# Optimization experiments

Hardware: AMD Instinct MI355X
Metric: run time of the kernel (lower is better)

Reference implementation:

```python
import jax, jax.numpy as jnp
import numpy as np

B, S, H = 2, 1024, 2048
NH, NKV, HD = 16, 4, 128
E, TOPK, I = 8, 2, 768
EPS = 1e-6
ROPE_THETA = 1000000.0


def setup_inputs() -> dict:
    key = jax.random.key(0)
    ks = jax.random.split(key, 14)
    sc = 0.02
    hidden_states = jax.random.normal(ks[0], (B, S, H), jnp.float32)
    # rotary embeddings (HF-style: cos/sin of shape [B, S, head_dim])
    pos = jnp.arange(S, dtype=jnp.float32)
    inv_freq = 1.0 / (ROPE_THETA ** (jnp.arange(0, HD, 2, dtype=jnp.float32) / HD))
    freqs = pos[:, None] * inv_freq[None, :]            # [S, HD/2]
    emb = jnp.concatenate([freqs, freqs], axis=-1)      # [S, HD]
    cos = jnp.broadcast_to(jnp.cos(emb)[None], (B, S, HD))
    sin = jnp.broadcast_to(jnp.sin(emb)[None], (B, S, HD))
    # additive causal mask [B, 1, S, S]
    causal = jnp.tril(jnp.ones((S, S), bool))
    attention_mask = jnp.broadcast_to(
        jnp.where(causal, 0.0, -1e9).astype(jnp.float32)[None, None], (B, 1, S, S))
    params = dict(
        w_q=jax.random.normal(ks[1], (NH * HD, H), jnp.float32) * sc,
        w_k=jax.random.normal(ks[2], (NKV * HD, H), jnp.float32) * sc,
        w_v=jax.random.normal(ks[3], (NKV * HD, H), jnp.float32) * sc,
        w_o=jax.random.normal(ks[4], (H, NH * HD), jnp.float32) * sc,
        q_norm_w=jnp.ones((HD,), jnp.float32),
        k_norm_w=jnp.ones((HD,), jnp.float32),
        ln1_w=jnp.ones((H,), jnp.float32),
        ln2_w=jnp.ones((H,), jnp.float32),
        gate_w=jax.random.normal(ks[5], (E, H), jnp.float32) * sc,
        w_gate_e=jax.random.normal(ks[6], (E, I, H), jnp.float32) * sc,
        w_up_e=jax.random.normal(ks[7], (E, I, H), jnp.float32) * sc,
        w_down_e=jax.random.normal(ks[8], (E, H, I), jnp.float32) * sc,
    )
    return dict(hidden_states=hidden_states, start_pos=0, cos=cos, sin=sin,
                attention_mask=attention_mask, **params)


def _rmsnorm(x, w):
    return x * jax.lax.rsqrt(jnp.mean(x * x, axis=-1, keepdims=True) + EPS) * w


def _rotate_half(x):
    x1, x2 = jnp.split(x, 2, axis=-1)
    return jnp.concatenate([-x2, x1], axis=-1)


def reference(hidden_states, start_pos, cos, sin, attention_mask,
              w_q, w_k, w_v, w_o, q_norm_w, k_norm_w, ln1_w, ln2_w,
              gate_w, w_gate_e, w_up_e, w_down_e):
    b, s, h = hidden_states.shape
    # ---- attention block ----
    x = _rmsnorm(hidden_states, ln1_w)
    q = _rmsnorm((x @ w_q.T).reshape(b, s, NH, HD), q_norm_w)
    k = _rmsnorm((x @ w_k.T).reshape(b, s, NKV, HD), k_norm_w)
    v = (x @ w_v.T).reshape(b, s, NKV, HD)
    c, sn = cos[:, :, None, :], sin[:, :, None, :]
    q = q * c + _rotate_half(q) * sn
    k = k * c + _rotate_half(k) * sn
    # GQA: repeat kv heads (start_pos=0 -> cache holds only current keys/values)
    rep = NH // NKV
    k = jnp.repeat(k, rep, axis=2)
    v = jnp.repeat(v, rep, axis=2)
    scale = HD ** -0.5
    scores = jnp.einsum('bqhd,bkhd->bhqk', q, k) * scale + attention_mask
    attn = jax.nn.softmax(scores, axis=-1)
    ctx = jnp.einsum('bhqk,bkhd->bqhd', attn, v).reshape(b, s, NH * HD)
    hidden_states = hidden_states + ctx @ w_o.T
    # ---- sparse MoE block ----
    x2 = _rmsnorm(hidden_states, ln2_w).reshape(-1, h)          # [T, H]
    logits = x2 @ gate_w.T                                      # [T, E]
    probs = jax.nn.softmax(logits.astype(jnp.float32), axis=-1)
    topw, topi = jax.lax.top_k(probs, TOPK)                     # [T, K]
    topw = topw / jnp.sum(topw, axis=-1, keepdims=True)         # norm_topk_prob
    # combine weights [T, E]: nonzero only on selected experts -> same math as
    # the original gather/scatter dispatch, expressed densely.
    cw = jnp.sum(jax.nn.one_hot(topi, E, dtype=x2.dtype) * topw[..., None], axis=1)
    g = jnp.einsum('th,eih->tei', x2, w_gate_e)                 # [T, E, I]
    u = jnp.einsum('th,eih->tei', x2, w_up_e)
    act = jax.nn.silu(g) * u
    moe_out = jnp.einsum('tei,ehi->th', act * cw[:, :, None], w_down_e)
    return hidden_states + moe_out.reshape(b, s, h)
```

## Files before the change

kernel.cpp:

```cpp
#include <hip/hip_runtime.h>


namespace {

constexpr int cB = 2, cS = 1024, cH = 2048;
constexpr int cNH = 16, cNKV = 4, cHD = 128;
constexpr int cE = 8, cI = 768;
constexpr int cT = cB * cS;
constexpr int cDq = cNH * cHD;
constexpr int cDkv = cNKV * cHD;
constexpr float cEPS = 1e-6f;
constexpr float cSCALE = 0.08838834764831845f;
constexpr int cQT = cS / 64;

typedef __attribute__((ext_vector_type(8))) short bf16x8;
typedef __attribute__((ext_vector_type(4))) float f32x4;

__device__ __forceinline__ unsigned pack2(float f0, float f1) {
  unsigned u0 = __float_as_uint(f0), u1 = __float_as_uint(f1);
  unsigned r0 = (u0 + (0x7FFFu + ((u0 >> 16) & 1u))) >> 16;
  unsigned r1 = (u1 + (0x7FFFu + ((u1 >> 16) & 1u))) & 0xFFFF0000u;
  return r0 | r1;
}
__device__ __forceinline__ uint4 pack8(const float4& a, const float4& b) {
  return make_uint4(pack2(a.x, a.y), pack2(a.z, a.w),
                    pack2(b.x, b.y), pack2(b.z, b.w));
}

__device__ __forceinline__ unsigned pack2t(float f0, float f1) {
  return (__float_as_uint(f0) >> 16) | (__float_as_uint(f1) & 0xFFFF0000u);
}
__device__ __forceinline__ float hi_of(float f) {
  return __uint_as_float(__float_as_uint(f) & 0xFFFF0000u);
}
__device__ __forceinline__ void split8(const float4& x, const float4& y,
                                       uint4& h, uint4& l) {
  h = make_uint4(pack2t(x.x, x.y), pack2t(x.z, x.w),
                 pack2t(y.x, y.y), pack2t(y.z, y.w));
  float l0 = x.x - hi_of(x.x), l1 = x.y - hi_of(x.y);
  float l2 = x.z - hi_of(x.z), l3 = x.w - hi_of(x.w);
  float l4 = y.x - hi_of(y.x), l5 = y.y - hi_of(y.y);
  float l6 = y.z - hi_of(y.z), l7 = y.w - hi_of(y.w);
  l = make_uint4(pack2t(l0, l1), pack2t(l2, l3), pack2t(l4, l5), pack2t(l6, l7));
}

__global__ __launch_bounds__(256) void k_rmsnorm(
    const float* __restrict__ xin, const float* __restrict__ w,
    float* __restrict__ y) {
  int t = blockIdx.x, tid = threadIdx.x;
  __shared__ float red[256];
  const float* xr = xin + (size_t)t * cH;
  float xv[8];
  float ss = 0.f;
#pragma unroll
  for (int i = 0; i < 8; ++i) {
    xv[i] = xr[tid + i * 256];
    ss += xv[i] * xv[i];
  }
  red[tid] = ss;
  __syncthreads();
  for (int s = 128; s > 0; s >>= 1) {
    if (tid < s) red[tid] += red[tid + s];
    __syncthreads();
  }
  float inv = rsqrtf(red[0] / (float)cH + cEPS);
#pragma unroll
  for (int i = 0; i < 8; ++i)
    y[(size_t)t * cH + tid + i * 256] = xv[i] * inv * w[tid + i * 256];
}

#define SGEMM_BODY(APTR_EXPR, WPTR_EXPR, KDIM, EPILOGUE)                      \
  __shared__ __align__(16) short Ah[128 * 32];                                \
  __shared__ __align__(16) short Al[128 * 32];                                \
  __shared__ __align__(16) short Bh[128 * 32];                                \
  __shared__ __align__(16) short Bl[128 * 32];                                \
  int tid = threadIdx.x;                                                      \
  int sdst[2];                                                                \
  const float* aptr[2];                                                       \
  const float* wptr[2];                                                       \
  _Pragma("unroll") for (int b2 = 0; b2 < 2; ++b2) {                          \
    int bid = tid + b2 * 256;                                                 \
    int row = bid >> 2, blk = bid & 3;                                        \
    sdst[b2] = row * 4 + (blk ^ ((row >> 1) & 3));                            \
    aptr[b2] = (APTR_EXPR) + blk * 8;                                         \
    wptr[b2] = (WPTR_EXPR) + blk * 8;                                         \
  }                                                                           \
  int w = tid >> 6, l = tid & 63;                                             \
  int wr = (w >> 1) * 64, wc = (w & 1) * 64;                                  \
  int sub = l >> 4, l16 = l & 15;                                             \
  int offA[4], offB[4];                                                       \
  _Pragma("unroll") for (int i = 0; i < 4; ++i) {                             \
    int ra = wr + i * 16 + l16;                                               \
    offA[i] = ra * 4 + (sub ^ ((ra >> 1) & 3));                               \
    int rb = wc + i * 16 + l16;                                               \
    offB[i] = rb * 4 + (sub ^ ((rb >> 1) & 3));                               \
  }                                                                           \
  f32x4 acc[4][4] = {};                                                       \
  uint4* Ah4 = (uint4*)Ah;                                                    \
  uint4* Al4 = (uint4*)Al;                                                    \
  uint4* Bh4 = (uint4*)Bh;                                                    \
  uint4* Bl4 = (uint4*)Bl;                                                    \
  const bf16x8* Ahf = (const bf16x8*)Ah;                                      \
  const bf16x8* Alf = (const bf16x8*)Al;                                      \
  const bf16x8* Bhf = (const bf16x8*)Bh;                                      \
  const bf16x8* Blf = (const bf16x8*)Bl;                                      \
  for (int k0 = 0; k0 < (KDIM); k0 += 32) {                                   \
    float4 av0[2], av1[2], wv0[2], wv1[2];                                    \
    _Pragma("unroll") for (int b2 = 0; b2 < 2; ++b2) {                        \
      av0[b2] = *(const float4*)(aptr[b2] + k0);                              \
      av1[b2] = *(const float4*)(aptr[b2] + k0 + 4);                          \
      wv0[b2] = *(const float4*)(wptr[b2] + k0);                              \
      wv1[b2] = *(const float4*)(wptr[b2] + k0 + 4);                          \
    }                                                                         \
    __syncthreads();                                                          \
    _Pragma("unroll") for (int b2 = 0; b2 < 2; ++b2) {                        \
      uint4 h, lo;                                                            \
      split8(av0[b2], av1[b2], h, lo);                                        \
      Ah4[sdst[b2]] = h;                                                      \
      Al4[sdst[b2]] = lo;                                                     \
      split8(wv0[b2], wv1[b2], h, lo);                                        \
      Bh4[sdst[b2]] = h;                                                      \
      Bl4[sdst[b2]] = lo;                                                     \
    }                                                                         \
    __syncthreads();                                                          \
    bf16x8 ah[4], al[4], bh[4], bl[4];                                        \
    _Pragma("unroll") for (int i = 0; i < 4; ++i) {                           \
      ah[i] = Ahf[offA[i]];                                                   \
      al[i] = Alf[offA[i]];                                                   \
    }                                                                         \
    _Pragma("unroll") for (int j = 0; j < 4; ++j) {                           \
      bh[j] = Bhf[offB[j]];                                                   \
      bl[j] = Blf[offB[j]];                                                   \
    }                                                                         \
    _Pragma("unroll") for (int i = 0; i < 4; ++i)                             \
        _Pragma("unroll") for (int j = 0; j < 4; ++j) {                       \
      acc[i][j] = __builtin_amdgcn_mfma_f32_16x16x32_bf16(ah[i], bh[j],       \
                                                          acc[i][j], 0, 0, 0);\
      acc[i][j] = __builtin_amdgcn_mfma_f32_16x16x32_bf16(al[i], bh[j],       \
                                                          acc[i][j], 0, 0, 0);\
      acc[i][j] = __builtin_amdgcn_mfma_f32_16x16x32_bf16(ah[i], bl[j],       \
                                                          acc[i][j], 0, 0, 0);\
    }                                                                         \
  }                                                                           \
  _Pragma("unroll") for (int i = 0; i < 4; ++i) {                             \
    _Pragma("unroll") for (int rr = 0; rr < 4; ++rr) {                        \
      int lr = wr + i * 16 + sub * 4 + rr;                                    \
      _Pragma("unroll") for (int j = 0; j < 4; ++j) {                         \
        int nn = wc + j * 16 + l16;                                           \
        float vv = acc[i][j][rr];                                             \
        EPILOGUE;                                                             \
      }                                                                       \
    }                                                                         \
  }

__global__ __launch_bounds__(256, 2) void k_sgemm_qkv(
    const float* __restrict__ A, const float* __restrict__ Wq,
    const float* __restrict__ Wk, const float* __restrict__ Wv,
    float* __restrict__ Cq, float* __restrict__ Ck, float* __restrict__ Cv) {
  int nBase = blockIdx.x * 128;
  int mBase = blockIdx.y * 128;
  const float* W;
  float* C;
  int Nout, ncol;
  if (nBase < cDq) {
    W = Wq; C = Cq; Nout = cDq; ncol = nBase;
  } else if (nBase < cDq + cDkv) {
    W = Wk; C = Ck; Nout = cDkv; ncol = nBase - cDq;
  } else {
    W = Wv; C = Cv; Nout = cDkv; ncol = nBase - cDq - cDkv;
  }
  SGEMM_BODY(A + (size_t)(mBase + row) * cH,
             W + (size_t)(ncol + row) * cH, cH,
             C[(size_t)(mBase + lr) * Nout + ncol + nn] = vv)
}

__global__ __launch_bounds__(256, 2) void k_sgemm_o(
    const float* __restrict__ A, const float* __restrict__ W,
    float* __restrict__ C, const float* __restrict__ resid) {
  int nBase = blockIdx.x * 128;
  int mBase = blockIdx.y * 128;
  SGEMM_BODY(A + (size_t)(mBase + row) * cH,
             W + (size_t)(nBase + row) * cH, cH,
             {
               size_t idx = (size_t)(mBase + lr) * cH + nBase + nn;
               C[idx] = vv + resid[idx];
             })
}

__global__ __launch_bounds__(128) void k_qknorm_rope(
    float* qbuf, float* kbuf,
    const float* __restrict__ qw, const float* __restrict__ kw,
    const float* __restrict__ cosb, const float* __restrict__ sinb,
    int cosBS) {
  int t = blockIdx.x, head = blockIdx.y, d = threadIdx.x;
  float* buf;
  const float* w;
  if (head < cNH) {
    buf = qbuf + (size_t)t * cDq + head * cHD;
    w = qw;
  } else {
    buf = kbuf + (size_t)t * cDkv + (head - cNH) * cHD;
    w = kw;
  }
  __shared__ float xs[cHD];
  __shared__ float red[cHD];
  float x = buf[d];
  xs[d] = x;
  red[d] = x * x;
  __syncthreads();
  for (int s = 64; s > 0; s >>= 1) {
    if (d < s) red[d] += red[d + s];
    __syncthreads();
  }
  float inv = rsqrtf(red[0] / (float)cHD + cEPS);
  int od = d ^ 64;
  float y = x * inv * w[d];
  float yo = xs[od] * inv * w[od];
  float rot = (d < 64) ? -yo : yo;
  size_t ci = (size_t)(t % cosBS) * cHD + d;
  buf[d] = y * cosb[ci] + rot * sinb[ci];
}

__device__ __forceinline__ int swzKQ(int r, int cb) {
  return r * 128 + ((cb ^ ((r >> 2) & 7)) << 2);
}

__global__ __launch_bounds__(256) void k_attn_tiled(
    float* qc, const float* __restrict__ k, const float* __restrict__ v) {
  __shared__ __align__(16) float Qs[64 * 128];
  __shared__ __align__(16) float KVs[64 * 128];
  int pidx = blockIdx.x, h = blockIdx.y, b = blockIdx.z;
  int kvh = h >> 2;
  int tid = threadIdx.x;
  int tx = tid & 15, ty = tid >> 4;
  const float* kbase = k + (size_t)b * cS * cDkv + kvh * cHD;
  const float* vbase = v + (size_t)b * cS * cDkv + kvh * cHD;
  float* qhbase = qc + (size_t)b * cS * cDq + h * cHD;

  for (int half = 0; half < 2; ++half) {
    int qt = half ? (cQT - 1 - pidx) : pidx;
#pragma unroll
    for (int ch = 0; ch < 8; ++ch) {
      int idx = tid + ch * 256;
      int r = idx >> 5, cb = idx & 31;
      float4 qv = *(const float4*)(qhbase + (size_t)(qt * 64 + r) * cDq + cb * 4);
      qv.x *= cSCALE; qv.y *= cSCALE; qv.z *= cSCALE; qv.w *= cSCALE;
      *(float4*)&Qs[swzKQ(r, cb)] = qv;
    }
    float4 kreg[8];
#pragma unroll
    for (int ch = 0; ch < 8; ++ch) {
      int idx = tid + ch * 256;
      int r = idx >> 5, cb = idx & 31;
      kreg[ch] = *(const float4*)(kbase + (size_t)r * cDkv + cb * 4);
    }
    float m[4], l[4], O[4][8];
#pragma unroll
    for (int i = 0; i < 4; ++i) {
      m[i] = -1e30f;
      l[i] = 0.f;
#pragma unroll
      for (int j = 0; j < 8; ++j) O[i][j] = 0.f;
    }
    __syncthreads();

    for (int kt = 0; kt <= qt; ++kt) {
#pragma unroll
      for (int ch = 0; ch < 8; ++ch) {
        int idx = tid + ch * 256;
        *(float4*)&KVs[swzKQ(idx >> 5, idx & 31)] = kreg[ch];
      }
      __syncthreads();
      float4 vreg[8];
#pragma unroll
      for (int ch = 0; ch < 8; ++ch) {
        int idx = tid + ch * 256;
        int r = idx >> 5, cb = idx & 31;
        vreg[ch] = *(const float4*)(vbase + (size_t)(kt * 64 + r) * cDkv + cb * 4);
      }
      float acc[4][4] = {};
#pragma unroll 8
      for (int dblk = 0; dblk < 32; ++dblk) {
        float4 a4[4], b4[4];
#pragma unroll
        for (int i = 0; i < 4; ++i)
          a4[i] = *(const float4*)&Qs[swzKQ(ty * 4 + i, dblk)];
#pragma unroll
        for (int j = 0; j < 4; ++j)
          b4[j] = *(const float4*)&KVs[swzKQ(tx * 4 + j, dblk)];
#pragma unroll
        for (int i = 0; i < 4; ++i)
#pragma unroll
          for (int j = 0; j < 4; ++j)
            acc[i][j] += a4[i].x * b4[j].x + a4[i].y * b4[j].y +
                         a4[i].z * b4[j].z + a4[i].w * b4[j].w;
      }
      if (kt == qt) {
#pragma unroll
        for (int i = 0; i < 4; ++i)
#pragma unroll
          for (int j = 0; j < 4; ++j)
            if (tx * 4 + j > ty * 4 + i) acc[i][j] = -1e30f;
      }
      float ps[4][4];
#pragma unroll
      for (int i = 0; i < 4; ++i) {
        float rm = fmaxf(fmaxf(acc[i][0], acc[i][1]), fmaxf(acc[i][2], acc[i][3]));
#pragma unroll
        for (int msk = 1; msk < 16; msk <<= 1) rm = fmaxf(rm, __shfl_xor(rm, msk));
        float nm = fmaxf(m[i], rm);
        float sc_ = __expf(m[i] - nm);
        float rs = 0.f;
#pragma unroll
        for (int j = 0; j < 4; ++j) {
          ps[i][j] = __expf(acc[i][j] - nm);
          rs += ps[i][j];
        }
#pragma unroll
        for (int msk = 1; msk < 16; msk <<= 1) rs += __shfl_xor(rs, msk);
        l[i] = l[i] * sc_ + rs;
        m[i] = nm;
#pragma unroll
        for (int j = 0; j < 8; ++j) O[i][j] *= sc_;
      }
      __syncthreads();
#pragma unroll
      for (int ch = 0; ch < 8; ++ch) {
        int idx = tid + ch * 256;
        *(float4*)&KVs[swzKQ(idx >> 5, idx & 31)] = vreg[ch];
      }
      __syncthreads();
      if (kt < qt) {
#pragma unroll
        for (int ch = 0; ch < 8; ++ch) {
          int idx = tid + ch * 256;
          int r = idx >> 5, cb = idx & 31;
          kreg[ch] =
              *(const float4*)(kbase + (size_t)((kt + 1) * 64 + r) * cDkv + cb * 4);
        }
      }
#pragma unroll
      for (int kc = 0; kc < 16; ++kc) {
        float4 va[4], vb[4];
#pragma unroll
        for (int q = 0; q < 4; ++q) {
          int kk = kc * 4 + q;
          va[q] = *(const float4*)&KVs[swzKQ(kk, tx)];
          vb[q] = *(const float4*)&KVs[swzKQ(kk, tx + 16)];
        }
        int src = (tid & 48) | kc;
#pragma unroll
        for (int q = 0; q < 4; ++q)
#pragma unroll
          for (int i = 0; i < 4; ++i) {
            float pq = __shfl(ps[i][q], src);
            O[i][0] += pq * va[q].x;
            O[i][1] += pq * va[q].y;
            O[i][2] += pq * va[q].z;
            O[i][3] += pq * va[q].w;
            O[i][4] += pq * vb[q].x;
            O[i][5] += pq * vb[q].y;
            O[i][6] += pq * vb[q].z;
            O[i][7] += pq * vb[q].w;
          }
      }
      __syncthreads();
    }
#pragma unroll
    for (int i = 0; i < 4; ++i) {
      float inv = 1.f / l[i];
      float* orow = qhbase + (size_t)(qt * 64 + ty * 4 + i) * cDq;
      *(float4*)(orow + tx * 4) =
          make_float4(O[i][0] * inv, O[i][1] * inv, O[i][2] * inv, O[i][3] * inv);
      *(float4*)(orow + 64 + tx * 4) =
          make_float4(O[i][4] * inv, O[i][5] * inv, O[i][6] * inv, O[i][7] * inv);
    }
  }
}

__global__ void k_zero_counts(int* __restrict__ counts) {
  if (threadIdx.x < cE) counts[threadIdx.x] = 0;
}

__global__ __launch_bounds__(64) void k_route(
    const float* __restrict__ x2, const float* __restrict__ gw,
    float* __restrict__ topw, int* __restrict__ counts, int* __restrict__ lists) {
  int t = blockIdx.x, lane = threadIdx.x;
  float acc[cE];
#pragma unroll
  for (int e = 0; e < cE; ++e) acc[e] = 0.f;
  const float* xr = x2 + (size_t)t * cH;
  for (int hh = lane; hh < cH; hh += 64) {
    float xv = xr[hh];
#pragma unroll
    for (int e = 0; e < cE; ++e) acc[e] += xv * gw[e * cH + hh];
  }
#pragma unroll
  for (int e = 0; e < cE; ++e)
    for (int off = 32; off > 0; off >>= 1) acc[e] += __shfl_down(acc[e], off);
  if (lane == 0) {
    int i0 = 0;
    float l0 = acc[0];
#pragma unroll
    for (int e = 1; e < cE; ++e)
      if (acc[e] > l0) { l0 = acc[e]; i0 = e; }
    int i1 = -1;
    float l1 = -1e30f;
#pragma unroll
    for (int e = 0; e < cE; ++e)
      if (e != i0 && acc[e] > l1) { l1 = acc[e]; i1 = e; }
    if (i1 < 0) { i1 = (i0 + 1) & 7; l1 = l0; }
    float r = expf(l1 - l0);
    topw[t * 2 + 0] = 1.f / (1.f + r);
    topw[t * 2 + 1] = r / (1.f + r);
    int p0 = atomicAdd(&counts[i0], 1);
    lists[i0 * cT + p0] = t * 2;
    int p1 = atomicAdd(&counts[i1], 1);
    lists[i1 * cT + p1] = t * 2 + 1;
  }
}

__global__ __launch_bounds__(256, 2) void k_mfma_gateup(
    const float* __restrict__ X, const float* __restrict__ Wg,
    const float* __restrict__ Wu, const int* __restrict__ counts,
    const int* __restrict__ lists, const float* __restrict__ topw,
    float* __restrict__ act) {
  int e = blockIdx.z;
  int cnt = counts[e];
  int mBase = blockIdx.y * 128;
  if (mBase >= cnt) return;
  int nBase = blockIdx.x * 128;
  __shared__ __align__(16) short As[128 * 32];
  __shared__ __align__(16) short Gs[128 * 32];
  __shared__ __align__(16) short Us[128 * 32];
  __shared__ int rowE[128];
  int tid = threadIdx.x;
  if (tid < 128) {
    int r = mBase + tid;
    rowE[tid] = (r < cnt) ? lists[e * cT + r] : -1;
  }
  __syncthreads();
  const float* gbase = Wg + (size_t)e * cI * cH;
  const float* ubase = Wu + (size_t)e * cI * cH;
  int sdst[2];
  const float* aptr[2];
  const float* gptr[2];
  const float* uptr[2];
#pragma unroll
  for (int b2 = 0; b2 < 2; ++b2) {
    int bid = tid + b2 * 256;
    int row = bid >> 2, blk = bid & 3;
    sdst[b2] = row * 4 + (blk ^ ((row >> 1) & 3));
    int ent = rowE[row];
    int arow = (ent < 0) ? 0 : (ent >> 1);
    aptr[b2] = X + (size_t)arow * cH + blk * 8;
    gptr[b2] = gbase + (size_t)(nBase + row) * cH + blk * 8;
    uptr[b2] = ubase + (size_t)(nBase + row) * cH + blk * 8;
  }
  int w = tid >> 6, l = tid & 63;
  int wr = (w >> 1) * 64, wc = (w & 1) * 64;
  int sub = l >> 4, l16 = l & 15;
  int offA[4], offB[4];
#pragma unroll
  for (int i = 0; i < 4; ++i) {
    int ra = wr + i * 16 + l16;
    offA[i] = ra * 4 + (sub ^ ((ra >> 1) & 3));
    int rb = wc + i * 16 + l16;
    offB[i] = rb * 4 + (sub ^ ((rb >> 1) & 3));
  }
  f32x4 accg[4][4] = {}, accu[4][4] = {};
  uint4* As4 = (uint4*)As;
  uint4* Gs4 = (uint4*)Gs;
  uint4* Us4 = (uint4*)Us;
  const bf16x8* Af = (const bf16x8*)As;
  const bf16x8* Gf = (const bf16x8*)Gs;
  const bf16x8* Uf = (const bf16x8*)Us;
  for (int k0 = 0; k0 < cH; k0 += 32) {
    float4 av0[2], av1[2], gv0[2], gv1[2], uv0[2], uv1[2];
#pragma unroll
    for (int b2 = 0; b2 < 2; ++b2) {
      av0[b2] = *(const float4*)(aptr[b2] + k0);
      av1[b2] = *(const float4*)(aptr[b2] + k0 + 4);
      gv0[b2] = *(const float4*)(gptr[b2] + k0);
      gv1[b2] = *(const float4*)(gptr[b2] + k0 + 4);
      uv0[b2] = *(const float4*)(uptr[b2] + k0);
      uv1[b2] = *(const float4*)(uptr[b2] + k0 + 4);
    }
    __syncthreads();
#pragma unroll
    for (int b2 = 0; b2 < 2; ++b2) {
      As4[sdst[b2]] = pack8(av0[b2], av1[b2]);
      Gs4[sdst[b2]] = pack8(gv0[b2], gv1[b2]);
      Us4[sdst[b2]] = pack8(uv0[b2], uv1[b2]);
    }
    __syncthreads();
    bf16x8 af[4];
#pragma unroll
    for (int i = 0; i < 4; ++i) af[i] = Af[offA[i]];
#pragma unroll
    for (int j = 0; j < 4; ++j) {
      bf16x8 bg = Gf[offB[j]];
      bf16x8 bu = Uf[offB[j]];
#pragma unroll
      for (int i = 0; i < 4; ++i) {
        accg[i][j] = __builtin_amdgcn_mfma_f32_16x16x32_bf16(
            af[i], bg, accg[i][j], 0, 0, 0);
        accu[i][j] = __builtin_amdgcn_mfma_f32_16x16x32_bf16(
            af[i], bu, accu[i][j], 0, 0, 0);
      }
    }
  }
#pragma unroll
  for (int i = 0; i < 4; ++i) {
#pragma unroll
    for (int rr = 0; rr < 4; ++rr) {
      int lr = wr + i * 16 + sub * 4 + rr;
      int ent = rowE[lr];
      if (ent < 0) continue;
      float wgt = topw[ent];
#pragma unroll
      for (int j = 0; j < 4; ++j) {
        int n = nBase + wc + j * 16 + l16;
        float g = accg[i][j][rr], u = accu[i][j][rr];
        float sg = g / (1.f + __expf(-g));
        act[(size_t)ent * cI + n] = sg * u * wgt;
      }
    }
  }
}

__global__ __launch_bounds__(256, 2) void k_mfma_down(
    const float* __restrict__ act, const float* __restrict__ Wd,
    const int* __restrict__ counts, const int* __restrict__ lists,
    float* __restrict__ F) {
  int e = blockIdx.z;
  int cnt = counts[e];
  int mBase = blockIdx.y * 128;
  if (mBase >= cnt) return;
  int nBase = blockIdx.x * 128;
  __shared__ __align__(16) short As[128 * 32];
  __shared__ __align__(16) short Bs[128 * 32];
  __shared__ int rowE[128];
  int tid = threadIdx.x;
  if (tid < 128) {
    int r = mBase + tid;
    rowE[tid] = (r < cnt) ? lists[e * cT + r] : -1;
  }
  __syncthreads();
  const float* wbase = Wd + (size_t)e * cH * cI;
  int sdst[2];
  const float* aptr[2];
  const float* wptr[2];
#pragma unroll
  for (int b2 = 0; b2 < 2; ++b2) {
    int bid = tid + b2 * 256;
    int row = bid >> 2, blk = bid & 3;
    sdst[b2] = row * 4 + (blk ^ ((row >> 1) & 3));
    int ent = rowE[row];
    int arow = (ent < 0) ? 0 : ent;
    aptr[b2] = act + (size_t)arow * cI + blk * 8;
    wptr[b2] = wbase + (size_t)(nBase + row) * cI + blk * 8;
  }
  int w = tid >> 6, l = tid & 63;
  int wr = (w >> 1) * 64, wc = (w & 1) * 64;
  int sub = l >> 4, l16 = l & 15;
  int offA[4], offB[4];
#pragma unroll
  for (int i = 0; i < 4; ++i) {
    int ra = wr + i * 16 + l16;
    offA[i] = ra * 4 + (sub ^ ((ra >> 1) & 3));
    int rb = wc + i * 16 + l16;
    offB[i] = rb * 4 + (sub ^ ((rb >> 1) & 3));
  }
  f32x4 acc[4][4] = {};
  uint4* As4 = (uint4*)As;
  uint4* Bs4 = (uint4*)Bs;
  const bf16x8* Af = (const bf16x8*)As;
  const bf16x8* Bf = (const bf16x8*)Bs;
  for (int k0 = 0; k0 < cI; k0 += 32) {
    float4 av0[2], av1[2], wv0[2], wv1[2];
#pragma unroll
    for (int b2 = 0; b2 < 2; ++b2) {
      av0[b2] = *(const float4*)(aptr[b2] + k0);
      av1[b2] = *(const float4*)(aptr[b2] + k0 + 4);
      wv0[b2] = *(const float4*)(wptr[b2] + k0);
      wv1[b2] = *(const float4*)(wptr[b2] + k0 + 4);
    }
    __syncthreads();
#pragma unroll
    for (int b2 = 0; b2 < 2; ++b2) {
      As4[sdst[b2]] = pack8(av0[b2], av1[b2]);
      Bs4[sdst[b2]] = pack8(wv0[b2], wv1[b2]);
    }
    __syncthreads();
    bf16x8 af[4], bfr[4];
#pragma unroll
    for (int i = 0; i < 4; ++i) af[i] = Af[offA[i]];
#pragma unroll
    for (int j = 0; j < 4; ++j) bfr[j] = Bf[offB[j]];
#pragma unroll
    for (int i = 0; i < 4; ++i)
#pragma unroll
      for (int j = 0; j < 4; ++j)
        acc[i][j] = __builtin_amdgcn_mfma_f32_16x16x32_bf16(
            af[i], bfr[j], acc[i][j], 0, 0, 0);
  }
#pragma unroll
  for (int i = 0; i < 4; ++i) {
#pragma unroll
    for (int rr = 0; rr < 4; ++rr) {
      int lr = wr + i * 16 + sub * 4 + rr;
      int ent = rowE[lr];
      if (ent < 0) continue;
      int t = ent >> 1;
#pragma unroll
      for (int j = 0; j < 4; ++j) {
        int n = nBase + wc + j * 16 + l16;
        atomicAdd(&F[(size_t)t * cH + n], acc[i][j][rr]);
      }
    }
  }
}

}

extern "C" void kernel_launch(void* const* d_in, const int* in_sizes, int n_in,
                              void* d_out, int out_size, void* d_ws, size_t ws_size,
                              hipStream_t stream) {
  (void)n_in; (void)out_size; (void)ws_size;
  int off = (in_sizes[1] == 1) ? 0 : -1;
  const float* hidden   = (const float*)d_in[0];
  const float* cosb     = (const float*)d_in[2 + off];
  const float* sinb     = (const float*)d_in[3 + off];
  const float* w_q      = (const float*)d_in[5 + off];
  const float* w_k      = (const float*)d_in[6 + off];
  const float* w_v      = (const float*)d_in[7 + off];
  const float* w_o      = (const float*)d_in[8 + off];
  const float* q_norm_w = (const float*)d_in[9 + off];
  const float* k_norm_w = (const float*)d_in[10 + off];
  const float* ln1_w    = (const float*)d_in[11 + off];
  const float* ln2_w    = (const float*)d_in[12 + off];
  const float* gate_w   = (const float*)d_in[13 + off];
  const float* w_gate_e = (const float*)d_in[14 + off];
  const float* w_up_e   = (const float*)d_in[15 + off];
  const float* w_down_e = (const float*)d_in[16 + off];
  float* F = (float*)d_out;
  int cosBS = in_sizes[2 + off] / cHD;

  float* ws = (float*)d_ws;
  float* xbuf  = ws;
  float* qcbuf = xbuf + (size_t)cT * cH;
  float* kbuf  = qcbuf + (size_t)cT * cDq;
  float* vbuf  = kbuf + (size_t)cT * cDkv;
  float* topw  = vbuf + (size_t)cT * cDkv;
  int* counts  = (int*)(topw + (size_t)cT * 2);
  int* lists   = counts + cE;
  float* act   = qcbuf;

  k_rmsnorm<<<cT, 256, 0, stream>>>(hidden, ln1_w, xbuf);
  k_sgemm_qkv<<<dim3((cDq + 2 * cDkv) / 128, cT / 128), 256, 0, stream>>>(
      xbuf, w_q, w_k, w_v, qcbuf, kbuf, vbuf);
  k_qknorm_rope<<<dim3(cT, cNH + cNKV), 128, 0, stream>>>(
      qcbuf, kbuf, q_norm_w, k_norm_w, cosb, sinb, cosBS);
  k_attn_tiled<<<dim3(cQT / 2, cNH, cB), 256, 0, stream>>>(qcbuf, kbuf, vbuf);
  k_sgemm_o<<<dim3(cH / 128, cT / 128), 256, 0, stream>>>(
      qcbuf, w_o, F, hidden);
  k_rmsnorm<<<cT, 256, 0, stream>>>(F, ln2_w, xbuf);
  k_zero_counts<<<1, 64, 0, stream>>>(counts);
  k_route<<<cT, 64, 0, stream>>>(xbuf, gate_w, topw, counts, lists);
  k_mfma_gateup<<<dim3(cI / 128, cT / 128, cE), 256, 0, stream>>>(
      xbuf, w_gate_e, w_up_e, counts, lists, topw, act);
  k_mfma_down<<<dim3(cH / 128, cT / 128, cE), 256, 0, stream>>>(
      act, w_down_e, counts, lists, F);
}
```

Measured before the change: 1.011 ms.

## Split attention blocks per query tile and stage probabilities through shared memory

The attention kernel no longer pairs a short and a long query tile in one block. It launches one block per (query tile, head, batch), and the 1D block index is ordered so that the first 256 blocks take the short tiles (qt 0..7) and the remaining 256 take the long tiles in descending order (qt 15..8). The P matrix is now written to a swizzled shared buffer and read back as float4, replacing the per-element cross-lane shuffles in the PV product. This doubles the block count for better occupancy and load balance, at the cost of an extra 16KB of LDS per block, which may lower residency, and one more shared-memory store/load round trip.

```diff
diff --git a/kernel.cpp b/kernel.cpp
--- a/kernel.cpp
+++ b/kernel.cpp
@@ -224,12 +224,26 @@
 __device__ __forceinline__ int swzKQ(int r, int cb) {
   return r * 128 + ((cb ^ ((r >> 2) & 7)) << 2);
 }
+__device__ __forceinline__ int swzP(int r, int cb) {
+  return r * 64 + ((cb ^ ((r >> 2) & 7)) << 2);
+}
 
 __global__ __launch_bounds__(256) void k_attn_tiled(
     float* qc, const float* __restrict__ k, const float* __restrict__ v) {
   __shared__ __align__(16) float Qs[64 * 128];
   __shared__ __align__(16) float KVs[64 * 128];
-  int pidx = blockIdx.x, h = blockIdx.y, b = blockIdx.z;
+  __shared__ __align__(16) float Ps[64 * 64];
+  int bid = blockIdx.x;
+  int qt, rest;
+  if (bid < 256) {
+    qt = bid >> 5;
+    rest = bid & 31;
+  } else {
+    int r2 = bid - 256;
+    qt = 15 - (r2 >> 5);
+    rest = r2 & 31;
+  }
+  int h = rest >> 1, b = rest & 1;
   int kvh = h >> 2;
   int tid = threadIdx.x;
   int tx = tid & 15, ty = tid >> 4;
@@ -237,144 +251,147 @@
   const float* vbase = v + (size_t)b * cS * cDkv + kvh * cHD;
   float* qhbase = qc + (size_t)b * cS * cDq + h * cHD;
 
-  for (int half = 0; half < 2; ++half) {
-    int qt = half ? (cQT - 1 - pidx) : pidx;
+#pragma unroll
+  for (int ch = 0; ch < 8; ++ch) {
+    int idx = tid + ch * 256;
+    int r = idx >> 5, cb = idx & 31;
+    float4 qv = *(const float4*)(qhbase + (size_t)(qt * 64 + r) * cDq + cb * 4);
+    qv.x *= cSCALE; qv.y *= cSCALE; qv.z *= cSCALE; qv.w *= cSCALE;
+    *(float4*)&Qs[swzKQ(r, cb)] = qv;
+  }
+  float4 kreg[8];
+#pragma unroll
+  for (int ch = 0; ch < 8; ++ch) {
+    int idx = tid + ch * 256;
+    int r = idx >> 5, cb = idx & 31;
+    kreg[ch] = *(const float4*)(kbase + (size_t)r * cDkv + cb * 4);
+  }
+  float m[4], l[4], O[4][8];
+#pragma unroll
+  for (int i = 0; i < 4; ++i) {
+    m[i] = -1e30f;
+    l[i] = 0.f;
+#pragma unroll
+    for (int j = 0; j < 8; ++j) O[i][j] = 0.f;
+  }
+  __syncthreads();
+
+  for (int kt = 0; kt <= qt; ++kt) {
+#pragma unroll
+    for (int ch = 0; ch < 8; ++ch) {
+      int idx = tid + ch * 256;
+      *(float4*)&KVs[swzKQ(idx >> 5, idx & 31)] = kreg[ch];
+    }
+    __syncthreads();
+    float4 vreg[8];
 #pragma unroll
     for (int ch = 0; ch < 8; ++ch) {
       int idx = tid + ch * 256;
       int r = idx >> 5, cb = idx & 31;
-      float4 qv = *(const float4*)(qhbase + (size_t)(qt * 64 + r) * cDq + cb * 4);
-      qv.x *= cSCALE; qv.y *= cSCALE; qv.z *= cSCALE; qv.w *= cSCALE;
-      *(float4*)&Qs[swzKQ(r, cb)] = qv;
-    }
-    float4 kreg[8];
+      vreg[ch] = *(const float4*)(vbase + (size_t)(kt * 64 + r) * cDkv + cb * 4);
+    }
+    float acc[4][4] = {};
+#pragma unroll 8
+    for (int dblk = 0; dblk < 32; ++dblk) {
+      float4 a4[4], b4[4];
+#pragma unroll
+      for (int i = 0; i < 4; ++i)
+        a4[i] = *(const float4*)&Qs[swzKQ(ty * 4 + i, dblk)];
+#pragma unroll
+      for (int j = 0; j < 4; ++j)
+        b4[j] = *(const float4*)&KVs[swzKQ(tx * 4 + j, dblk)];
+#pragma unroll
+      for (int i = 0; i < 4; ++i)
+#pragma unroll
+        for (int j = 0; j < 4; ++j)
+          acc[i][j] += a4[i].x * b4[j].x + a4[i].y * b4[j].y +
+                       a4[i].z * b4[j].z + a4[i].w * b4[j].w;
+    }
+    if (kt == qt) {
+#pragma unroll
+      for (int i = 0; i < 4; ++i)
+#pragma unroll
+        for (int j = 0; j < 4; ++j)
+          if (tx * 4 + j > ty * 4 + i) acc[i][j] = -1e30f;
+    }
+    float ps[4][4];
+#pragma unroll
+    for (int i = 0; i < 4; ++i) {
+      float rm = fmaxf(fmaxf(acc[i][0], acc[i][1]), fmaxf(acc[i][2], acc[i][3]));
+#pragma unroll
+      for (int msk = 1; msk < 16; msk <<= 1) rm = fmaxf(rm, __shfl_xor(rm, msk));
+      float nm = fmaxf(m[i], rm);
+      float sc_ = __expf(m[i] - nm);
+      float rs = 0.f;
+#pragma unroll
+      for (int j = 0; j < 4; ++j) {
+        ps[i][j] = __expf(acc[i][j] - nm);
+        rs += ps[i][j];
+      }
+#pragma unroll
+      for (int msk = 1; msk < 16; msk <<= 1) rs += __shfl_xor(rs, msk);
+      l[i] = l[i] * sc_ + rs;
+      m[i] = nm;
+#pragma unroll
+      for (int j = 0; j < 8; ++j) O[i][j] *= sc_;
+    }
+    __syncthreads();
 #pragma unroll
     for (int ch = 0; ch < 8; ++ch) {
       int idx = tid + ch * 256;
-      int r = idx >> 5, cb = idx & 31;
-      kreg[ch] = *(const float4*)(kbase + (size_t)r * cDkv + cb * 4);
-    }
-    float m[4], l[4], O[4][8];
-#pragma unroll
-    for (int i = 0; i < 4; ++i) {
-      m[i] = -1e30f;
-      l[i] = 0.f;
-#pragma unroll
-      for (int j = 0; j < 8; ++j) O[i][j] = 0.f;
-    }
-    __syncthreads();
-
-    for (int kt = 0; kt <= qt; ++kt) {
-#pragma unroll
-      for (int ch = 0; ch < 8; ++ch) {
-        int idx = tid + ch * 256;
-        *(float4*)&KVs[swzKQ(idx >> 5, idx & 31)] = kreg[ch];
-      }
-      __syncthreads();
-      float4 vreg[8];
+      *(float4*)&KVs[swzKQ(idx >> 5, idx & 31)] = vreg[ch];
+    }
+#pragma unroll
+    for (int i = 0; i < 4; ++i)
+      *(float4*)&Ps[swzP(ty * 4 + i, tx)] =
+          make_float4(ps[i][0], ps[i][1], ps[i][2], ps[i][3]);
+    __syncthreads();
+    if (kt < qt) {
 #pragma unroll
       for (int ch = 0; ch < 8; ++ch) {
         int idx = tid + ch * 256;
         int r = idx >> 5, cb = idx & 31;
-        vreg[ch] = *(const float4*)(vbase + (size_t)(kt * 64 + r) * cDkv + cb * 4);
+        kreg[ch] =
+            *(const float4*)(kbase + (size_t)((kt + 1) * 64 + r) * cDkv + cb * 4);
       }
-      float acc[4][4] = {};
-#pragma unroll 8
-      for (int dblk = 0; dblk < 32; ++dblk) {
-        float4 a4[4], b4[4];
-#pragma unroll
-        for (int i = 0; i < 4; ++i)
-          a4[i] = *(const float4*)&Qs[swzKQ(ty * 4 + i, dblk)];
-#pragma unroll
-        for (int j = 0; j < 4; ++j)
-          b4[j] = *(const float4*)&KVs[swzKQ(tx * 4 + j, dblk)];
-#pragma unroll
-        for (int i = 0; i < 4; ++i)
-#pragma unroll
-          for (int j = 0; j < 4; ++j)
-            acc[i][j] += a4[i].x * b4[j].x + a4[i].y * b4[j].y +
-                         a4[i].z * b4[j].z + a4[i].w * b4[j].w;
+    }
+#pragma unroll 4
+    for (int kc = 0; kc < 16; ++kc) {
+      float4 p4[4];
+#pragma unroll
+      for (int i = 0; i < 4; ++i)
+        p4[i] = *(const float4*)&Ps[swzP(ty * 4 + i, kc)];
+      float pv_[4][4];
+#pragma unroll
+      for (int i = 0; i < 4; ++i) {
+        pv_[i][0] = p4[i].x; pv_[i][1] = p4[i].y;
+        pv_[i][2] = p4[i].z; pv_[i][3] = p4[i].w;
       }
-      if (kt == qt) {
-#pragma unroll
-        for (int i = 0; i < 4; ++i)
-#pragma unroll
-          for (int j = 0; j < 4; ++j)
-            if (tx * 4 + j > ty * 4 + i) acc[i][j] = -1e30f;
-      }
-      float ps[4][4];
-#pragma unroll
-      for (int i = 0; i < 4; ++i) {
-        float rm = fmaxf(fmaxf(acc[i][0], acc[i][1]), fmaxf(acc[i][2], acc[i][3]));
-#pragma unroll
-        for (int msk = 1; msk < 16; msk <<= 1) rm = fmaxf(rm, __shfl_xor(rm, msk));
-        float nm = fmaxf(m[i], rm);
-        float sc_ = __expf(m[i] - nm);
-        float rs = 0.f;
-#pragma unroll
-        for (int j = 0; j < 4; ++j) {
-          ps[i][j] = __expf(acc[i][j] - nm);
-          rs += ps[i][j];
-        }
-#pragma unroll
-        for (int msk = 1; msk < 16; msk <<= 1) rs += __shfl_xor(rs, msk);
-        l[i] = l[i] * sc_ + rs;
-        m[i] = nm;
-#pragma unroll
-        for (int j = 0; j < 8; ++j) O[i][j] *= sc_;
-      }
-      __syncthreads();
-#pragma unroll
-      for (int ch = 0; ch < 8; ++ch) {
-        int idx = tid + ch * 256;
-        *(float4*)&KVs[swzKQ(idx >> 5, idx & 31)] = vreg[ch];
-      }
-      __syncthreads();
-      if (kt < qt) {
-#pragma unroll
-        for (int ch = 0; ch < 8; ++ch) {
-          int idx = tid + ch * 256;
-          int r = idx >> 5, cb = idx & 31;
-          kreg[ch] =
-              *(const float4*)(kbase + (size_t)((kt + 1) * 64 + r) * cDkv + cb * 4);
+#pragma unroll
+      for (int q = 0; q < 4; ++q) {
+        int kk = kc * 4 + q;
+        float4 va = *(const float4*)&KVs[swzKQ(kk, tx)];
+        float4 vb = *(const float4*)&KVs[swzKQ(kk, tx + 16)];
+#pragma unroll
+        for (int i = 0; i < 4; ++i) {
+          float pq = pv_[i][q];
+          O[i][0] += pq * va.x; O[i][1] += pq * va.y;
+          O[i][2] += pq * va.z; O[i][3] += pq * va.w;
+          O[i][4] += pq * vb.x; O[i][5] += pq * vb.y;
+          O[i][6] += pq * vb.z; O[i][7] += pq * vb.w;
         }
       }
-#pragma unroll
-      for (int kc = 0; kc < 16; ++kc) {
-        float4 va[4], vb[4];
-#pragma unroll
-        for (int q = 0; q < 4; ++q) {
-          int kk = kc * 4 + q;
-          va[q] = *(const float4*)&KVs[swzKQ(kk, tx)];
-          vb[q] = *(const float4*)&KVs[swzKQ(kk, tx + 16)];
-        }
-        int src = (tid & 48) | kc;
-#pragma unroll
-        for (int q = 0; q < 4; ++q)
-#pragma unroll
-          for (int i = 0; i < 4; ++i) {
-            float pq = __shfl(ps[i][q], src);
-            O[i][0] += pq * va[q].x;
-            O[i][1] += pq * va[q].y;
-            O[i][2] += pq * va[q].z;
-            O[i][3] += pq * va[q].w;
-            O[i][4] += pq * vb[q].x;
-            O[i][5] += pq * vb[q].y;
-            O[i][6] += pq * vb[q].z;
-            O[i][7] += pq * vb[q].w;
-          }
-      }
-      __syncthreads();
-    }
-#pragma unroll
-    for (int i = 0; i < 4; ++i) {
-      float inv = 1.f / l[i];
-      float* orow = qhbase + (size_t)(qt * 64 + ty * 4 + i) * cDq;
-      *(float4*)(orow + tx * 4) =
-          make_float4(O[i][0] * inv, O[i][1] * inv, O[i][2] * inv, O[i][3] * inv);
-      *(float4*)(orow + 64 + tx * 4) =
-          make_float4(O[i][4] * inv, O[i][5] * inv, O[i][6] * inv, O[i][7] * inv);
-    }
+    }
+    __syncthreads();
+  }
+#pragma unroll
+  for (int i = 0; i < 4; ++i) {
+    float inv = 1.f / l[i];
+    float* orow = qhbase + (size_t)(qt * 64 + ty * 4 + i) * cDq;
+    *(float4*)(orow + tx * 4) =
+        make_float4(O[i][0] * inv, O[i][1] * inv, O[i][2] * inv, O[i][3] * inv);
+    *(float4*)(orow + 64 + tx * 4) =
+        make_float4(O[i][4] * inv, O[i][5] * inv, O[i][6] * inv, O[i][7] * inv);
   }
 }
 
@@ -662,7 +679,7 @@
       xbuf, w_q, w_k, w_v, qcbuf, kbuf, vbuf);
   k_qknorm_rope<<<dim3(cT, cNH + cNKV), 128, 0, stream>>>(
       qcbuf, kbuf, q_norm_w, k_norm_w, cosb, sinb, cosBS);
-  k_attn_tiled<<<dim3(cQT / 2, cNH, cB), 256, 0, stream>>>(qcbuf, kbuf, vbuf);
+  k_attn_tiled<<<2 * cQT * cNH * cB / 2, 256, 0, stream>>>(qcbuf, kbuf, vbuf);
   k_sgemm_o<<<dim3(cH / 128, cT / 128), 256, 0, stream>>>(
       qcbuf, w_o, F, hidden);
   k_rmsnorm<<<cT, 256, 0, stream>>>(F, ln2_w, xbuf);
```

Measured after the change: 1.000 ms. No clear change (-1.1%).
